# Optimization experiments

Measured on AMD Instinct MI355X. Metric: run time of the kernel, lower is better.

The kernel has to match this reference:

```python
import jax, jax.numpy as jnp
import numpy as np

B, S, E, H = 2, 2048, 512, 8
D = E // H  # head size = 64
LN_EPS = 1e-5


def setup_inputs() -> dict:
    key = jax.random.key(0)
    ks = jax.random.split(key, 8)
    s_in = 1.0 / np.sqrt(E)
    return {
        "x": jax.random.normal(ks[0], (B, S, E), jnp.float32),
        # per-head projection weights, stored [H, E, D] so q = x @ Wq[h]
        "Wq": jax.random.normal(ks[1], (H, E, D), jnp.float32) * s_in,
        "Wk": jax.random.normal(ks[2], (H, E, D), jnp.float32) * s_in,
        "Wv": jax.random.normal(ks[3], (H, E, D), jnp.float32) * s_in,
        "Wp": jax.random.normal(ks[4], (E, E), jnp.float32) * s_in,
        "bp": jnp.zeros((E,), jnp.float32),
        "gamma": jnp.ones((E,), jnp.float32),
        "beta": jnp.zeros((E,), jnp.float32),
        # causal mask buffer: masked_fill where mask == 0
        "mask": jnp.tril(jnp.ones((S, S), jnp.int32)),
    }


def reference(x, Wq, Wk, Wv, Wp, bp, gamma, beta, mask):
    # batched per-head projections (equivalent to the H small Linears)
    q = jnp.einsum("bse,hed->bhsd", x, Wq)
    k = jnp.einsum("bse,hed->bhsd", x, Wk)
    v = jnp.einsum("bse,hed->bhsd", x, Wv)
    # NOTE: original has NO 1/sqrt(d) scaling
    att_log = jnp.einsum("bhsd,bhtd->bhst", q, k)
    att_log = jnp.where(mask == 0, -jnp.inf, att_log)
    att = jax.nn.softmax(att_log, axis=-1)
    o = jnp.einsum("bhst,bhtd->bhsd", att, v)  # [B,H,S,D]
    # torch.cat((val, values)) prepends each head -> final order head H-1 .. 0
    o = o[:, ::-1]
    vals = o.transpose(0, 2, 1, 3).reshape(B, S, E)
    out = vals @ Wp.T + bp + x
    mu = jnp.mean(out, axis=-1, keepdims=True)
    var = jnp.var(out, axis=-1, keepdims=True)
    return (out - mu) * jax.lax.rsqrt(var + LN_EPS) * gamma + beta
```

## Files before the change

kernel.cpp:

```cpp
#include <hip/hip_runtime.h>

constexpr int Bn = 2;
constexpr int Sn = 2048;
constexpr int En = 512;
constexpr int Hn = 8;
constexpr int Dn = 64;
constexpr int Mn = Bn * Sn;

typedef short bf8 __attribute__((ext_vector_type(8)));
typedef float f32x4 __attribute__((ext_vector_type(4)));

constexpr size_t XY = (size_t)Mn * En;
constexpr size_t WT = (size_t)3 * En * En;
constexpr size_t WP = (size_t)En * En;
constexpr size_t PL = (size_t)Bn * Hn * Sn * Dn;

__device__ __forceinline__ unsigned short f2bf(float f) {
    unsigned int u = __float_as_uint(f);
    unsigned int r = 0x7FFFu + ((u >> 16) & 1u);
    return (unsigned short)((u + r) >> 16);
}
__device__ __forceinline__ float bf2f(unsigned short u) {
    return __uint_as_float(((unsigned int)u) << 16);
}
__device__ __forceinline__ void split2(float f, unsigned short& hi, unsigned short& lo) {
    hi = f2bf(f);
    lo = f2bf(f - bf2f(hi));
}

__global__ __launch_bounds__(256)
void presplit(const float* __restrict__ src,
              unsigned short* __restrict__ hi_p,
              unsigned short* __restrict__ lo_p)
{
    const size_t base = ((size_t)blockIdx.x * 256 + threadIdx.x) * 8;
    float a[8];
    *(float4*)&a[0] = *(const float4*)(src + base);
    *(float4*)&a[4] = *(const float4*)(src + base + 4);
    unsigned short h[8], l[8];
    #pragma unroll
    for (int j = 0; j < 8; ++j) split2(a[j], h[j], l[j]);
    *(bf8*)(hi_p + base) = *(bf8*)&h[0];
    *(bf8*)(lo_p + base) = *(bf8*)&l[0];
}

__global__ __launch_bounds__(256)
void split_wt(const float* __restrict__ Wq,
              const float* __restrict__ Wk,
              const float* __restrict__ Wv,
              unsigned short* __restrict__ Wth,
              unsigned short* __restrict__ Wtl)
{
    __shared__ float t[64][65];
    const int ph = blockIdx.x;
    const int proj = ph >> 3, h = ph & 7;
    const int e0 = blockIdx.y * 64;
    const int tid = threadIdx.x;
    const float* W = (proj == 0) ? Wq : (proj == 1) ? Wk : Wv;
    const float* src = W + (size_t)h * En * Dn + (size_t)e0 * Dn;

    const int er = tid >> 2, cg = (tid & 3) * 16;
    #pragma unroll
    for (int c = 0; c < 4; ++c) {
        float4 v = *(const float4*)(src + (size_t)er * Dn + cg + 4 * c);
        t[er][cg + 4 * c + 0] = v.x;
        t[er][cg + 4 * c + 1] = v.y;
        t[er][cg + 4 * c + 2] = v.z;
        t[er][cg + 4 * c + 3] = v.w;
    }
    __syncthreads();

    const int d = tid >> 2, jg = (tid & 3) * 16;
    unsigned short h16[16], l16[16];
    #pragma unroll
    for (int j = 0; j < 16; ++j) split2(t[jg + j][d], h16[j], l16[j]);
    const size_t n = (size_t)proj * 512 + h * 64 + d;
    unsigned short* dh = Wth + n * En + e0 + jg;
    unsigned short* dl = Wtl + n * En + e0 + jg;
    *(bf8*)dh       = *(bf8*)&h16[0];
    *(bf8*)(dh + 8) = *(bf8*)&h16[8];
    *(bf8*)dl       = *(bf8*)&l16[0];
    *(bf8*)(dl + 8) = *(bf8*)&l16[8];
}

__global__ __launch_bounds__(256)
void qkv_gemm(const unsigned short* __restrict__ xh,
              const unsigned short* __restrict__ xl,
              const unsigned short* __restrict__ Wth,
              const unsigned short* __restrict__ Wtl,
              unsigned short* __restrict__ qh_g,
              unsigned short* __restrict__ ql_g,
              unsigned short* __restrict__ kh_g,
              unsigned short* __restrict__ kl_g,
              unsigned short* __restrict__ vT_g)
{
    __shared__ unsigned short Ah[128][40], Al[128][40];
    __shared__ unsigned short Bh[128][40], Bl[128][40];

    const int tid = threadIdx.x;
    const int m0 = blockIdx.x * 128;
    const int n0 = blockIdx.y * 128;
    const int proj = n0 >> 9;
    const int within = n0 & 511;

    const int wave = tid >> 6, lane = tid & 63;
    const int wm = (wave >> 1) * 64, wn = (wave & 1) * 64;
    const int lm = lane & 15, quad = lane >> 4;

    const int am = tid >> 1;
    const int aks = (tid & 1) * 16;
    const unsigned short* arh = xh + (size_t)(m0 + am) * En + aks;
    const unsigned short* arl = xl + (size_t)(m0 + am) * En + aks;

    const int nn = tid & 127;
    const int bkg = (tid >> 7) * 16;
    const unsigned short* brh = Wth + (size_t)(n0 + nn) * En + bkg;
    const unsigned short* brl = Wtl + (size_t)(n0 + nn) * En + bkg;

    f32x4 acc[4][4];
    #pragma unroll
    for (int i = 0; i < 4; ++i)
        #pragma unroll
        for (int j = 0; j < 4; ++j) acc[i][j] = (f32x4){0.f, 0.f, 0.f, 0.f};

    for (int k0 = 0; k0 < En; k0 += 32) {
        *(bf8*)&Ah[am][aks]     = *(const bf8*)(arh + k0);
        *(bf8*)&Ah[am][aks + 8] = *(const bf8*)(arh + k0 + 8);
        *(bf8*)&Al[am][aks]     = *(const bf8*)(arl + k0);
        *(bf8*)&Al[am][aks + 8] = *(const bf8*)(arl + k0 + 8);
        *(bf8*)&Bh[nn][bkg]     = *(const bf8*)(brh + k0);
        *(bf8*)&Bh[nn][bkg + 8] = *(const bf8*)(brh + k0 + 8);
        *(bf8*)&Bl[nn][bkg]     = *(const bf8*)(brl + k0);
        *(bf8*)&Bl[nn][bkg + 8] = *(const bf8*)(brl + k0 + 8);
        __syncthreads();

        bf8 a_h[4], a_l[4], b_h[4], b_l[4];
        #pragma unroll
        for (int mi = 0; mi < 4; ++mi) {
            a_h[mi] = *(const bf8*)&Ah[wm + mi * 16 + lm][quad * 8];
            a_l[mi] = *(const bf8*)&Al[wm + mi * 16 + lm][quad * 8];
        }
        #pragma unroll
        for (int ni = 0; ni < 4; ++ni) {
            b_h[ni] = *(const bf8*)&Bh[wn + ni * 16 + lm][quad * 8];
            b_l[ni] = *(const bf8*)&Bl[wn + ni * 16 + lm][quad * 8];
        }
        #pragma unroll
        for (int mi = 0; mi < 4; ++mi)
            #pragma unroll
            for (int ni = 0; ni < 4; ++ni) {
                acc[mi][ni] = __builtin_amdgcn_mfma_f32_16x16x32_bf16(a_h[mi], b_h[ni], acc[mi][ni], 0, 0, 0);
                acc[mi][ni] = __builtin_amdgcn_mfma_f32_16x16x32_bf16(a_h[mi], b_l[ni], acc[mi][ni], 0, 0, 0);
                acc[mi][ni] = __builtin_amdgcn_mfma_f32_16x16x32_bf16(a_l[mi], b_h[ni], acc[mi][ni], 0, 0, 0);
            }
        __syncthreads();
    }

    if (proj < 2) {
        unsigned short* hp = (proj == 0) ? qh_g : kh_g;
        unsigned short* lp = (proj == 0) ? ql_g : kl_g;
        #pragma unroll
        for (int mi = 0; mi < 4; ++mi) {
            #pragma unroll
            for (int r = 0; r < 4; ++r) {
                const int m = m0 + wm + mi * 16 + quad * 4 + r;
                const int b = m >> 11, s = m & 2047;
                #pragma unroll
                for (int ni = 0; ni < 4; ++ni) {
                    const int nl = within + wn + ni * 16 + lm;
                    const int h = nl >> 6, d = nl & 63;
                    const size_t idx = (((size_t)(b * Hn + h) * Sn + s) * Dn) + d;
                    unsigned short hv, lv;
                    split2(acc[mi][ni][r], hv, lv);
                    hp[idx] = hv;
                    lp[idx] = lv;
                }
            }
        }
    } else {
        #pragma unroll
        for (int mi = 0; mi < 4; ++mi) {
            const int s0 = m0 + wm + mi * 16 + quad * 4;
            const int b = s0 >> 11, s = s0 & 2047;
            #pragma unroll
            for (int ni = 0; ni < 4; ++ni) {
                const int nl = within + wn + ni * 16 + lm;
                const int h = nl >> 6, d = nl & 63;
                ushort4 pk;
                pk.x = f2bf(acc[mi][ni][0]);
                pk.y = f2bf(acc[mi][ni][1]);
                pk.z = f2bf(acc[mi][ni][2]);
                pk.w = f2bf(acc[mi][ni][3]);
                *(ushort4*)(vT_g + ((size_t)(b * Hn + h) * Dn + d) * Sn + s) = pk;
            }
        }
    }
}

__global__ __launch_bounds__(256)
void attn(const unsigned short* __restrict__ qh_g,
          const unsigned short* __restrict__ ql_g,
          const unsigned short* __restrict__ kh_g,
          const unsigned short* __restrict__ kl_g,
          const unsigned short* __restrict__ vT_g,
          float* __restrict__ vals)
{
    extern __shared__ unsigned short sm[];
    unsigned short (*khs)[72] = (unsigned short(*)[72])(sm);
    unsigned short (*kls)[72] = (unsigned short(*)[72])(sm + 4608);
    unsigned short (*vTs)[72] = (unsigned short(*)[72])(sm + 9216);
    unsigned short (*pts)[72] = (unsigned short(*)[72])(sm + 13824);
    float* alf  = (float*)(sm + 18432);
    float* linv = alf + 64;

    const int bidx = blockIdx.x;
    const int jj_ = bidx >> 4;
    const int bh = bidx & 15;
    const int qt = (jj_ < 16) ? jj_ : 47 - jj_;
    const int b = bh >> 3, h = bh & 7;
    const int tid = threadIdx.x;
    const int wave = tid >> 6, lane = tid & 63;
    const int quad = lane >> 4, lq = lane & 15;

    const unsigned short* khb = kh_g + (size_t)bh * Sn * Dn;
    const unsigned short* klb = kl_g + (size_t)bh * Sn * Dn;
    const unsigned short* vTb = vT_g + (size_t)bh * Dn * Sn;

    bf8 qfh[2], qfl[2];
    {
        const size_t qoff = ((size_t)bh * Sn + (size_t)qt * 64 + wave * 16 + lq) * Dn;
        #pragma unroll
        for (int c = 0; c < 2; ++c) {
            qfh[c] = *(const bf8*)(qh_g + qoff + c * 32 + quad * 8);
            qfl[c] = *(const bf8*)(ql_g + qoff + c * 32 + quad * 8);
        }
    }

    f32x4 accO[4];
    #pragma unroll
    for (int nj = 0; nj < 4; ++nj) accO[nj] = (f32x4){0.f, 0.f, 0.f, 0.f};
    float m = -INFINITY, l = 0.f;

    const int srow = tid & 63;
    const int sdg  = tid >> 6;

    const int ntk = qt + 1;
    for (int it = 0; it < ntk; ++it) {
        const int t0 = it * 64;
        __syncthreads();
        {
            const unsigned short* kr = khb + (size_t)(t0 + srow) * Dn + sdg * 16;
            const unsigned short* lr = klb + (size_t)(t0 + srow) * Dn + sdg * 16;
            const unsigned short* vr = vTb + (size_t)srow * Sn + t0 + sdg * 16;
            *(bf8*)&khs[srow][sdg * 16]     = *(const bf8*)(kr);
            *(bf8*)&khs[srow][sdg * 16 + 8] = *(const bf8*)(kr + 8);
            *(bf8*)&kls[srow][sdg * 16]     = *(const bf8*)(lr);
            *(bf8*)&kls[srow][sdg * 16 + 8] = *(const bf8*)(lr + 8);
            *(bf8*)&vTs[srow][sdg * 16]     = *(const bf8*)(vr);
            *(bf8*)&vTs[srow][sdg * 16 + 8] = *(const bf8*)(vr + 8);
        }
        __syncthreads();

        f32x4 accS[4];
        #pragma unroll
        for (int mi = 0; mi < 4; ++mi) accS[mi] = (f32x4){0.f, 0.f, 0.f, 0.f};
        #pragma unroll
        for (int mi = 0; mi < 4; ++mi) {
            #pragma unroll
            for (int c = 0; c < 2; ++c) {
                bf8 ah = *(const bf8*)&khs[mi * 16 + lq][c * 32 + quad * 8];
                bf8 al = *(const bf8*)&kls[mi * 16 + lq][c * 32 + quad * 8];
                accS[mi] = __builtin_amdgcn_mfma_f32_16x16x32_bf16(ah, qfh[c], accS[mi], 0, 0, 0);
                accS[mi] = __builtin_amdgcn_mfma_f32_16x16x32_bf16(ah, qfl[c], accS[mi], 0, 0, 0);
                accS[mi] = __builtin_amdgcn_mfma_f32_16x16x32_bf16(al, qfh[c], accS[mi], 0, 0, 0);
            }
        }

        if (it == qt) {
            const int qrel = wave * 16 + lq;
            #pragma unroll
            for (int mi = 0; mi < 4; ++mi)
                #pragma unroll
                for (int r = 0; r < 4; ++r)
                    if (mi * 16 + quad * 4 + r > qrel) accS[mi][r] = -INFINITY;
        }

        float mt = -INFINITY;
        #pragma unroll
        for (int mi = 0; mi < 4; ++mi)
            #pragma unroll
            for (int r = 0; r < 4; ++r) mt = fmaxf(mt, accS[mi][r]);
        mt = fmaxf(mt, __shfl_xor(mt, 16));
        mt = fmaxf(mt, __shfl_xor(mt, 32));
        const float mnew = fmaxf(m, mt);
        const float alpha = __expf(m - mnew);
        float ls = 0.f;
        #pragma unroll
        for (int mi = 0; mi < 4; ++mi)
            #pragma unroll
            for (int r = 0; r < 4; ++r) {
                const float p = __expf(accS[mi][r] - mnew);
                accS[mi][r] = p;
                ls += p;
            }
        ls += __shfl_xor(ls, 16);
        ls += __shfl_xor(ls, 32);
        l = l * alpha + ls;
        m = mnew;

        #pragma unroll
        for (int mi = 0; mi < 4; ++mi) {
            ushort4 pk;
            pk.x = f2bf(accS[mi][0]);
            pk.y = f2bf(accS[mi][1]);
            pk.z = f2bf(accS[mi][2]);
            pk.w = f2bf(accS[mi][3]);
            *(ushort4*)&pts[wave * 16 + lq][mi * 16 + quad * 4] = pk;
        }
        if (quad == 0) alf[wave * 16 + lq] = alpha;

        {
            float4 al4 = *(const float4*)&alf[wave * 16 + quad * 4];
            #pragma unroll
            for (int nj = 0; nj < 4; ++nj) {
                accO[nj][0] *= al4.x;
                accO[nj][1] *= al4.y;
                accO[nj][2] *= al4.z;
                accO[nj][3] *= al4.w;
            }
            #pragma unroll
            for (int c = 0; c < 2; ++c) {
                bf8 pf = *(const bf8*)&pts[wave * 16 + lq][c * 32 + quad * 8];
                #pragma unroll
                for (int nj = 0; nj < 4; ++nj) {
                    bf8 vf = *(const bf8*)&vTs[nj * 16 + lq][c * 32 + quad * 8];
                    accO[nj] = __builtin_amdgcn_mfma_f32_16x16x32_bf16(pf, vf, accO[nj], 0, 0, 0);
                }
            }
        }
    }

    if (quad == 0) linv[wave * 16 + lq] = 1.f / l;
    float4 li4 = *(const float4*)&linv[wave * 16 + quad * 4];
    const float lir[4] = {li4.x, li4.y, li4.z, li4.w};

    #pragma unroll
    for (int r = 0; r < 4; ++r) {
        const int s = qt * 64 + wave * 16 + quad * 4 + r;
        float* dst = vals + ((size_t)(b * Sn + s)) * En + (size_t)(7 - h) * 64;
        #pragma unroll
        for (int nj = 0; nj < 4; ++nj)
            dst[nj * 16 + lq] = accO[nj][r] * lir[r];
    }
}

__global__ __launch_bounds__(256)
void out_gemm(const float* __restrict__ vals,
              const unsigned short* __restrict__ Wph,
              const unsigned short* __restrict__ Wpl,
              const float* __restrict__ bp,
              const float* __restrict__ x,
              float* __restrict__ outp)
{
    __shared__ unsigned short Ah[64][40], Al[64][40];
    __shared__ unsigned short Bh[128][40], Bl[128][40];

    const int tid = threadIdx.x;
    const int m0 = blockIdx.x * 64;
    const int n0 = blockIdx.y * 128;

    const int wave = tid >> 6, lane = tid & 63;
    const int wm = (wave >> 1) * 32, wn = (wave & 1) * 64;
    const int lm = lane & 15, quad = lane >> 4;

    const int am = tid >> 2;
    const int aks = (tid & 3) * 8;
    const float* arow = vals + (size_t)(m0 + am) * En + aks;

    const int bn = tid >> 1;
    const int bks = (tid & 1) * 16;
    const unsigned short* brh = Wph + (size_t)(n0 + bn) * En + bks;
    const unsigned short* brl = Wpl + (size_t)(n0 + bn) * En + bks;

    f32x4 acc[2][4];
    #pragma unroll
    for (int i = 0; i < 2; ++i)
        #pragma unroll
        for (int j = 0; j < 4; ++j) acc[i][j] = (f32x4){0.f, 0.f, 0.f, 0.f};

    for (int k0 = 0; k0 < En; k0 += 32) {
        {
            float av[8];
            *(float4*)&av[0] = *(const float4*)(arow + k0);
            *(float4*)&av[4] = *(const float4*)(arow + k0 + 4);
            unsigned short hi[8], lo[8];
            #pragma unroll
            for (int j = 0; j < 8; ++j) split2(av[j], hi[j], lo[j]);
            *(bf8*)&Ah[am][aks] = *(bf8*)&hi[0];
            *(bf8*)&Al[am][aks] = *(bf8*)&lo[0];
        }
        *(bf8*)&Bh[bn][bks]     = *(const bf8*)(brh + k0);
        *(bf8*)&Bh[bn][bks + 8] = *(const bf8*)(brh + k0 + 8);
        *(bf8*)&Bl[bn][bks]     = *(const bf8*)(brl + k0);
        *(bf8*)&Bl[bn][bks + 8] = *(const bf8*)(brl + k0 + 8);
        __syncthreads();

        bf8 a_h[2], a_l[2], b_h[4], b_l[4];
        #pragma unroll
        for (int mi = 0; mi < 2; ++mi) {
            a_h[mi] = *(const bf8*)&Ah[wm + mi * 16 + lm][quad * 8];
            a_l[mi] = *(const bf8*)&Al[wm + mi * 16 + lm][quad * 8];
        }
        #pragma unroll
        for (int ni = 0; ni < 4; ++ni) {
            b_h[ni] = *(const bf8*)&Bh[wn + ni * 16 + lm][quad * 8];
            b_l[ni] = *(const bf8*)&Bl[wn + ni * 16 + lm][quad * 8];
        }
        #pragma unroll
        for (int mi = 0; mi < 2; ++mi)
            #pragma unroll
            for (int ni = 0; ni < 4; ++ni) {
                acc[mi][ni] = __builtin_amdgcn_mfma_f32_16x16x32_bf16(a_h[mi], b_h[ni], acc[mi][ni], 0, 0, 0);
                acc[mi][ni] = __builtin_amdgcn_mfma_f32_16x16x32_bf16(a_h[mi], b_l[ni], acc[mi][ni], 0, 0, 0);
                acc[mi][ni] = __builtin_amdgcn_mfma_f32_16x16x32_bf16(a_l[mi], b_h[ni], acc[mi][ni], 0, 0, 0);
            }
        __syncthreads();
    }

    #pragma unroll
    for (int mi = 0; mi < 2; ++mi) {
        #pragma unroll
        for (int r = 0; r < 4; ++r) {
            const int m = m0 + wm + mi * 16 + quad * 4 + r;
            #pragma unroll
            for (int ni = 0; ni < 4; ++ni) {
                const int n = n0 + wn + ni * 16 + lm;
                const size_t idx = (size_t)m * En + n;
                outp[idx] = acc[mi][ni][r] + bp[n] + x[idx];
            }
        }
    }
}

__global__ __launch_bounds__(256)
void ln_kernel(const float* __restrict__ outp,
               const float* __restrict__ gamma,
               const float* __restrict__ beta,
               float* __restrict__ y)
{
    const int row = blockIdx.x;
    const int tid = threadIdx.x;
    const float* r = outp + (size_t)row * En;

    const float a = r[tid];
    const float b = r[tid + 256];
    float sum = a + b;
    float sq = a * a + b * b;
    #pragma unroll
    for (int off = 32; off > 0; off >>= 1) {
        sum += __shfl_down(sum, off);
        sq  += __shfl_down(sq, off);
    }
    __shared__ float ls[4], lq[4];
    const int wid = tid >> 6, lane = tid & 63;
    if (lane == 0) { ls[wid] = sum; lq[wid] = sq; }
    __syncthreads();
    if (tid == 0) {
        float S = 0.f, Q = 0.f;
        #pragma unroll
        for (int w = 0; w < 4; ++w) { S += ls[w]; Q += lq[w]; }
        ls[0] = S; lq[0] = Q;
    }
    __syncthreads();
    const float mu = ls[0] * (1.f / 512.f);
    const float var = lq[0] * (1.f / 512.f) - mu * mu;
    const float rs = rsqrtf(var + 1e-5f);

    float* yr = y + (size_t)row * En;
    yr[tid]       = (a - mu) * rs * gamma[tid]       + beta[tid];
    yr[tid + 256] = (b - mu) * rs * gamma[tid + 256] + beta[tid + 256];
}

extern "C" void kernel_launch(void* const* d_in, const int* in_sizes, int n_in,
                              void* d_out, int out_size, void* d_ws, size_t ws_size,
                              hipStream_t stream)
{
    const float* x     = (const float*)d_in[0];
    const float* Wq    = (const float*)d_in[1];
    const float* Wk    = (const float*)d_in[2];
    const float* Wv    = (const float*)d_in[3];
    const float* Wp    = (const float*)d_in[4];
    const float* bp    = (const float*)d_in[5];
    const float* gamma = (const float*)d_in[6];
    const float* beta  = (const float*)d_in[7];

    float* ws   = (float*)d_ws;
    float* vals = ws;
    float* outp = ws + XY;
    unsigned short* bfb = (unsigned short*)(ws + 2 * XY);
    unsigned short* xh  = bfb;
    unsigned short* xl  = bfb + XY;
    unsigned short* Wth = bfb + 2 * XY;
    unsigned short* Wtl = Wth + WT;
    unsigned short* Wph = Wtl + WT;
    unsigned short* Wpl = Wph + WP;
    unsigned short* qh  = Wpl + WP;
    unsigned short* ql  = qh + PL;
    unsigned short* kh  = ql + PL;
    unsigned short* kl  = kh + PL;
    unsigned short* vT  = kl + PL;

    const int attn_lds = 18432 * 2 + 512;
    hipFuncSetAttribute((const void*)attn,
                        hipFuncAttributeMaxDynamicSharedMemorySize, attn_lds);

    presplit<<<dim3((int)(XY / (256 * 8))), 256, 0, stream>>>(x, xh, xl);
    presplit<<<dim3((int)(WP / (256 * 8))), 256, 0, stream>>>(Wp, Wph, Wpl);
    split_wt<<<dim3(24, 8), 256, 0, stream>>>(Wq, Wk, Wv, Wth, Wtl);
    qkv_gemm<<<dim3(Mn / 128, 12), 256, 0, stream>>>(xh, xl, Wth, Wtl,
                                                     qh, ql, kh, kl, vT);
    attn<<<dim3(512), 256, attn_lds, stream>>>(qh, ql, kh, kl, vT, vals);
    out_gemm<<<dim3(Mn / 64, En / 128), 256, 0, stream>>>(vals, Wph, Wpl, bp, x, outp);
    ln_kernel<<<dim3(Mn), 256, 0, stream>>>(outp, gamma, beta, (float*)d_out);
}
```

Measured before the change: 211.6 us.

## Split attention KV range across two blocks, combine partials, prefetch tiles, merge prep kernels

Each query tile's causal KV range is split into two halves processed by separate blocks, doubling the grid to 1024 blocks. Each block writes unnormalized bf16 partial outputs plus its running max and sum, and a new combine kernel merges the two halves. The attention loop now loads the next K/V tile into registers while the current tile is computed, and the three split kernels are fused into one prep launch. The aim is better occupancy and load balance on the long causal rows and less launch overhead. The cost is an extra kernel pass and bf16 rounding of the partial outputs before they are combined.

After: 184.5 us. 12.8% less time.

```diff
diff --git a/kernel.cpp b/kernel.cpp
--- a/kernel.cpp
+++ b/kernel.cpp
@@ -29,33 +29,38 @@
 }
 
 __global__ __launch_bounds__(256)
-void presplit(const float* __restrict__ src,
-              unsigned short* __restrict__ hi_p,
-              unsigned short* __restrict__ lo_p)
-{
-    const size_t base = ((size_t)blockIdx.x * 256 + threadIdx.x) * 8;
-    float a[8];
-    *(float4*)&a[0] = *(const float4*)(src + base);
-    *(float4*)&a[4] = *(const float4*)(src + base + 4);
-    unsigned short h[8], l[8];
-    #pragma unroll
-    for (int j = 0; j < 8; ++j) split2(a[j], h[j], l[j]);
-    *(bf8*)(hi_p + base) = *(bf8*)&h[0];
-    *(bf8*)(lo_p + base) = *(bf8*)&l[0];
-}
-
-__global__ __launch_bounds__(256)
-void split_wt(const float* __restrict__ Wq,
-              const float* __restrict__ Wk,
-              const float* __restrict__ Wv,
-              unsigned short* __restrict__ Wth,
-              unsigned short* __restrict__ Wtl)
+void prep(const float* __restrict__ x, const float* __restrict__ Wp,
+          const float* __restrict__ Wq, const float* __restrict__ Wk,
+          const float* __restrict__ Wv,
+          unsigned short* __restrict__ xh, unsigned short* __restrict__ xl,
+          unsigned short* __restrict__ Wph, unsigned short* __restrict__ Wpl,
+          unsigned short* __restrict__ Wth, unsigned short* __restrict__ Wtl)
 {
     __shared__ float t[64][65];
-    const int ph = blockIdx.x;
+    const int bid = blockIdx.x;
+    const int tid = threadIdx.x;
+
+    if (bid < 1152) {
+        const float* src = (bid < 1024) ? x : Wp;
+        unsigned short* hp = (bid < 1024) ? xh : Wph;
+        unsigned short* lp = (bid < 1024) ? xl : Wpl;
+        const int blk = (bid < 1024) ? bid : (bid - 1024);
+        const size_t base = ((size_t)blk * 256 + tid) * 8;
+        float a[8];
+        *(float4*)&a[0] = *(const float4*)(src + base);
+        *(float4*)&a[4] = *(const float4*)(src + base + 4);
+        unsigned short h[8], l[8];
+        #pragma unroll
+        for (int j = 0; j < 8; ++j) split2(a[j], h[j], l[j]);
+        *(bf8*)(hp + base) = *(bf8*)&h[0];
+        *(bf8*)(lp + base) = *(bf8*)&l[0];
+        return;
+    }
+
+    const int idx = bid - 1152;
+    const int ph = idx >> 3;
     const int proj = ph >> 3, h = ph & 7;
-    const int e0 = blockIdx.y * 64;
-    const int tid = threadIdx.x;
+    const int e0 = (idx & 7) * 64;
     const float* W = (proj == 0) ? Wq : (proj == 1) ? Wk : Wv;
     const float* src = W + (size_t)h * En * Dn + (size_t)e0 * Dn;
 
@@ -203,21 +208,26 @@
           const unsigned short* __restrict__ kh_g,
           const unsigned short* __restrict__ kl_g,
           const unsigned short* __restrict__ vT_g,
-          float* __restrict__ vals)
+          unsigned short* __restrict__ Op,
+          float* __restrict__ ml)
 {
     extern __shared__ unsigned short sm[];
     unsigned short (*khs)[72] = (unsigned short(*)[72])(sm);
     unsigned short (*kls)[72] = (unsigned short(*)[72])(sm + 4608);
     unsigned short (*vTs)[72] = (unsigned short(*)[72])(sm + 9216);
     unsigned short (*pts)[72] = (unsigned short(*)[72])(sm + 13824);
-    float* alf  = (float*)(sm + 18432);
-    float* linv = alf + 64;
+    float* alf = (float*)(sm + 18432);
 
     const int bidx = blockIdx.x;
-    const int jj_ = bidx >> 4;
-    const int bh = bidx & 15;
-    const int qt = (jj_ < 16) ? jj_ : 47 - jj_;
-    const int b = bh >> 3, h = bh & 7;
+    const int r_ = bidx & 255, quarter = bidx >> 8;
+    const int a_ = r_ >> 4, bh = r_ & 15;
+    const int qt = (quarter & 1) ? (31 - a_) : a_;
+    const int hf = quarter >> 1;
+    const int n0 = (qt + 2) >> 1;
+    const int its = hf ? n0 : 0;
+    const int ite = hf ? (qt + 1) : n0;
+    const int pslot = hf * 512 + bh * 32 + qt;
+
     const int tid = threadIdx.x;
     const int wave = tid >> 6, lane = tid & 63;
     const int quad = lane >> 4, lq = lane & 15;
@@ -239,27 +249,41 @@
     f32x4 accO[4];
     #pragma unroll
     for (int nj = 0; nj < 4; ++nj) accO[nj] = (f32x4){0.f, 0.f, 0.f, 0.f};
-    float m = -INFINITY, l = 0.f;
+    float m = -1e30f, l = 0.f;
 
     const int srow = tid & 63;
     const int sdg  = tid >> 6;
 
-    const int ntk = qt + 1;
-    for (int it = 0; it < ntk; ++it) {
-        const int t0 = it * 64;
+    bf8 pk0, pk1, pl0, pl1, pv0, pv1;
+    if (its < ite) {
+        const int t0 = its * 64;
+        const unsigned short* kr = khb + (size_t)(t0 + srow) * Dn + sdg * 16;
+        const unsigned short* lr = klb + (size_t)(t0 + srow) * Dn + sdg * 16;
+        const unsigned short* vr = vTb + (size_t)srow * Sn + t0 + sdg * 16;
+        pk0 = *(const bf8*)(kr);  pk1 = *(const bf8*)(kr + 8);
+        pl0 = *(const bf8*)(lr);  pl1 = *(const bf8*)(lr + 8);
+        pv0 = *(const bf8*)(vr);  pv1 = *(const bf8*)(vr + 8);
+    }
+
+    for (int it = its; it < ite; ++it) {
         __syncthreads();
-        {
-            const unsigned short* kr = khb + (size_t)(t0 + srow) * Dn + sdg * 16;
-            const unsigned short* lr = klb + (size_t)(t0 + srow) * Dn + sdg * 16;
-            const unsigned short* vr = vTb + (size_t)srow * Sn + t0 + sdg * 16;
-            *(bf8*)&khs[srow][sdg * 16]     = *(const bf8*)(kr);
-            *(bf8*)&khs[srow][sdg * 16 + 8] = *(const bf8*)(kr + 8);
-            *(bf8*)&kls[srow][sdg * 16]     = *(const bf8*)(lr);
-            *(bf8*)&kls[srow][sdg * 16 + 8] = *(const bf8*)(lr + 8);
-            *(bf8*)&vTs[srow][sdg * 16]     = *(const bf8*)(vr);
-            *(bf8*)&vTs[srow][sdg * 16 + 8] = *(const bf8*)(vr + 8);
-        }
+        *(bf8*)&khs[srow][sdg * 16]     = pk0;
+        *(bf8*)&khs[srow][sdg * 16 + 8] = pk1;
+        *(bf8*)&kls[srow][sdg * 16]     = pl0;
+        *(bf8*)&kls[srow][sdg * 16 + 8] = pl1;
+        *(bf8*)&vTs[srow][sdg * 16]     = pv0;
+        *(bf8*)&vTs[srow][sdg * 16 + 8] = pv1;
         __syncthreads();
+
+        if (it + 1 < ite) {
+            const int t1 = (it + 1) * 64;
+            const unsigned short* kr = khb + (size_t)(t1 + srow) * Dn + sdg * 16;
+            const unsigned short* lr = klb + (size_t)(t1 + srow) * Dn + sdg * 16;
+            const unsigned short* vr = vTb + (size_t)srow * Sn + t1 + sdg * 16;
+            pk0 = *(const bf8*)(kr);  pk1 = *(const bf8*)(kr + 8);
+            pl0 = *(const bf8*)(lr);  pl1 = *(const bf8*)(lr + 8);
+            pv0 = *(const bf8*)(vr);  pv1 = *(const bf8*)(vr + 8);
+        }
 
         f32x4 accS[4];
         #pragma unroll
@@ -340,18 +364,57 @@
         }
     }
 
-    if (quad == 0) linv[wave * 16 + lq] = 1.f / l;
-    float4 li4 = *(const float4*)&linv[wave * 16 + quad * 4];
-    const float lir[4] = {li4.x, li4.y, li4.z, li4.w};
-
+    if (quad == 0) {
+        const size_t mi_ = ((size_t)pslot * 64 + wave * 16 + lq) * 2;
+        ml[mi_]     = m;
+        ml[mi_ + 1] = l;
+    }
     #pragma unroll
     for (int r = 0; r < 4; ++r) {
-        const int s = qt * 64 + wave * 16 + quad * 4 + r;
-        float* dst = vals + ((size_t)(b * Sn + s)) * En + (size_t)(7 - h) * 64;
+        const int q = wave * 16 + quad * 4 + r;
+        unsigned short* dst = Op + ((size_t)pslot * 64 + q) * 64;
         #pragma unroll
         for (int nj = 0; nj < 4; ++nj)
-            dst[nj * 16 + lq] = accO[nj][r] * lir[r];
-    }
+            dst[nj * 16 + lq] = f2bf(accO[nj][r]);
+    }
+}
+
+__global__ __launch_bounds__(256)
+void attn_combine(const unsigned short* __restrict__ Op,
+                  const float* __restrict__ ml,
+                  float* __restrict__ vals)
+{
+    const int bq = blockIdx.x;
+    const int bh = bq >> 5, qt = bq & 31;
+    const int b = bh >> 3, h = bh & 7;
+    const int t = threadIdx.x;
+    const int q = t >> 2, dg = (t & 3) * 16;
+
+    const size_t p0 = (size_t)bq * 64 + q;
+    const size_t p1 = (size_t)(512 + bq) * 64 + q;
+    const float m0 = ml[p0 * 2], l0 = ml[p0 * 2 + 1];
+    const float m1 = ml[p1 * 2], l1 = ml[p1 * 2 + 1];
+    const float mn = fmaxf(m0, m1);
+    const float a0 = __expf(m0 - mn), a1 = __expf(m1 - mn);
+    const float inv = 1.f / (a0 * l0 + a1 * l1);
+
+    unsigned short o0[16], o1[16];
+    *(bf8*)&o0[0] = *(const bf8*)(Op + p0 * 64 + dg);
+    *(bf8*)&o0[8] = *(const bf8*)(Op + p0 * 64 + dg + 8);
+    *(bf8*)&o1[0] = *(const bf8*)(Op + p1 * 64 + dg);
+    *(bf8*)&o1[8] = *(const bf8*)(Op + p1 * 64 + dg + 8);
+
+    float out[16];
+    #pragma unroll
+    for (int j = 0; j < 16; ++j)
+        out[j] = (a0 * bf2f(o0[j]) + a1 * bf2f(o1[j])) * inv;
+
+    float* dst = vals + ((size_t)(b * Sn + qt * 64 + q)) * En
+                 + (size_t)(7 - h) * 64 + dg;
+    *(float4*)(dst)      = *(float4*)&out[0];
+    *(float4*)(dst + 4)  = *(float4*)&out[4];
+    *(float4*)(dst + 8)  = *(float4*)&out[8];
+    *(float4*)(dst + 12) = *(float4*)&out[12];
 }
 
 __global__ __launch_bounds__(256)
@@ -509,17 +572,19 @@
     unsigned short* kh  = ql + PL;
     unsigned short* kl  = kh + PL;
     unsigned short* vT  = kl + PL;
-
-    const int attn_lds = 18432 * 2 + 512;
+    unsigned short* Op = xh;
+    float* ml = outp;
+
+    const int attn_lds = 18432 * 2 + 256;
     hipFuncSetAttribute((const void*)attn,
                         hipFuncAttributeMaxDynamicSharedMemorySize, attn_lds);
 
-    presplit<<<dim3((int)(XY / (256 * 8))), 256, 0, stream>>>(x, xh, xl);
-    presplit<<<dim3((int)(WP / (256 * 8))), 256, 0, stream>>>(Wp, Wph, Wpl);
-    split_wt<<<dim3(24, 8), 256, 0, stream>>>(Wq, Wk, Wv, Wth, Wtl);
+    prep<<<dim3(1344), 256, 0, stream>>>(x, Wp, Wq, Wk, Wv,
+                                         xh, xl, Wph, Wpl, Wth, Wtl);
     qkv_gemm<<<dim3(Mn / 128, 12), 256, 0, stream>>>(xh, xl, Wth, Wtl,
                                                      qh, ql, kh, kl, vT);
-    attn<<<dim3(512), 256, attn_lds, stream>>>(qh, ql, kh, kl, vT, vals);
+    attn<<<dim3(1024), 256, attn_lds, stream>>>(qh, ql, kh, kl, vT, Op, ml);
+    attn_combine<<<dim3(512), 256, 0, stream>>>(Op, ml, vals);
     out_gemm<<<dim3(Mn / 64, En / 128), 256, 0, stream>>>(vals, Wph, Wpl, bp, x, outp);
     ln_kernel<<<dim3(Mn), 256, 0, stream>>>(outp, gamma, beta, (float*)d_out);
 }
```
